# Kernel tuning notes

Hardware: AMD Instinct MI355X
Metric: run time of the kernel (lower is better)

Reference implementation:

```python
import jax, jax.numpy as jnp
import numpy as np

B, S, DIM = 2, 2048, 2048
N_HEADS, N_KV_HEADS = 16, 8
HEAD_DIM = DIM // N_HEADS          # 128
KV_DIM = N_KV_HEADS * HEAD_DIM     # 1024
SKETCH = 64
ROPE_THETA = 500000.0
INV_SQRT_HD = np.float32(1.0 / np.sqrt(HEAD_DIM))


def sketch_mm(A, Sm, Bm):
    """projection_sketch_mm: approximate A @ Bm as (A S / k) @ (S^T B).
    A: (b, n, d), Sm: (b, d, k), Bm: (d, m)."""
    AS = jnp.matmul(A, Sm) / Sm.shape[-1]      # (b, n, k)
    SB = jnp.einsum('bdk,dm->bkm', Sm, Bm)     # (b, k, m)
    return jnp.matmul(AS, SB)                  # (b, n, m)


def apply_rotary(x, freqs_cis):
    """Faithful port of the module's apply_rotary_emb for one tensor.
    x: (b, s, h, hd); freqs_cis: (s, hd//2, 2) with [...,0]=cos, [...,1]=sin."""
    x2 = x.reshape(*x.shape[:-1], HEAD_DIM // 2, 2)
    f = freqs_cis[None, :, None, :, :]         # broadcast over batch & heads
    c, s = f[..., 0], f[..., 1]
    x0, x1 = x2[..., 0], x2[..., 1]
    row1 = x0 * c + x1 * s                     # dot(x, [cos, sin])
    row0 = x0 * s - x1 * c                     # dot(x, [sin, -cos]) (flip + negate)
    return jnp.stack([row0, row1], axis=-1).reshape(x.shape)


def setup_inputs() -> dict:
    key = jax.random.key(0)
    ks = jax.random.split(key, 9)
    x = jax.random.normal(ks[0], (B, S, DIM), jnp.float32)
    wq = jax.random.normal(ks[1], (DIM, DIM), jnp.float32) / np.float32(np.sqrt(DIM))
    wk = jax.random.normal(ks[2], (KV_DIM, DIM), jnp.float32) / np.float32(np.sqrt(DIM))
    wv = jax.random.normal(ks[3], (KV_DIM, DIM), jnp.float32) / np.float32(np.sqrt(DIM))
    wo = jax.random.normal(ks[4], (DIM, DIM), jnp.float32) / np.float32(np.sqrt(DIM))
    # gaussian sketch matrices (sketch_mode='gaussian'), one per batch element
    Sq = jax.random.normal(ks[5], (B, DIM, SKETCH), jnp.float32)
    Sk = jax.random.normal(ks[6], (B, DIM, SKETCH), jnp.float32)
    Sv = jax.random.normal(ks[7], (B, DIM, SKETCH), jnp.float32)
    So = jax.random.normal(ks[8], (B, DIM, SKETCH), jnp.float32)
    # RoPE table: (S, HEAD_DIM//2, 2) = stack([cos, sin])
    pos = jnp.arange(S, dtype=jnp.float32)
    inv = 1.0 / (ROPE_THETA ** (jnp.arange(0, HEAD_DIM, 2, dtype=jnp.float32) / HEAD_DIM))
    ang = pos[:, None] * inv[None, :]
    freqs_cis = jnp.stack([jnp.cos(ang), jnp.sin(ang)], axis=-1)
    return {"x": x, "wq": wq, "wk": wk, "wv": wv, "wo": wo,
            "Sq": Sq, "Sk": Sk, "Sv": Sv, "So": So, "freqs_cis": freqs_cis}


def reference(x, wq, wk, wv, wo, Sq, Sk, Sv, So, freqs_cis):
    b, s, _ = x.shape
    # RLALinear projections via projection sketch (weight stored (out, in) -> use W.T)
    xq = sketch_mm(x, Sq, wq.T).reshape(b, s, N_HEADS, HEAD_DIM)
    xk = sketch_mm(x, Sk, wk.T).reshape(b, s, N_KV_HEADS, HEAD_DIM)
    xv = sketch_mm(x, Sv, wv.T).reshape(b, s, N_KV_HEADS, HEAD_DIM)
    xq = apply_rotary(xq, freqs_cis)
    xk = apply_rotary(xk, freqs_cis)
    # repeat_kv: each kv head repeated n_rep times consecutively
    n_rep = N_HEADS // N_KV_HEADS
    k = jnp.repeat(xk, n_rep, axis=2)
    v = jnp.repeat(xv, n_rep, axis=2)
    q = xq.transpose(0, 2, 1, 3)               # (b, h, s, d)
    k = k.transpose(0, 2, 1, 3)
    v = v.transpose(0, 2, 1, 3)
    scores = jnp.einsum('bhqd,bhkd->bhqk', q, k) * INV_SQRT_HD
    mask = jnp.tril(jnp.ones((s, s), dtype=bool))
    scores = jnp.where(mask[None, None], scores, jnp.finfo(scores.dtype).min)
    probs = jax.nn.softmax(scores, axis=-1)
    out = jnp.einsum('bhqk,bhkd->bhqd', probs, v)
    out = out.transpose(0, 2, 1, 3).reshape(b, s, DIM)
    # output RLALinear via sketch
    return sketch_mm(out, So, wo.T)
```

## Files before the change

### kernel.cpp

```cpp
#include <hip/hip_runtime.h>
#include <math.h>

#define S_LEN 2048
#define DIM   2048
#define NH    16
#define NKV   8
#define HD    128
#define SKETCH 64
#define KV_DIM 1024
#define SCALE (0.08838834764831845f * 1.4426950408889634f)

typedef _Float16 half8_t  __attribute__((ext_vector_type(8)));
typedef __bf16   bf8_t    __attribute__((ext_vector_type(8)));
typedef __bf16   bf4_t    __attribute__((ext_vector_type(4)));
typedef float    f32x16_t __attribute__((ext_vector_type(16)));
typedef unsigned int uint4_t __attribute__((ext_vector_type(4)));

__global__ __launch_bounds__(256) void sbas_mfma(
    const float* __restrict__ x,
    const float* __restrict__ Sq, const float* __restrict__ Sk,
    const float* __restrict__ Sv, const float* __restrict__ So,
    const float* __restrict__ wq, const float* __restrict__ wk,
    const float* __restrict__ wv, const float* __restrict__ wo,
    float* __restrict__ SBq, float* __restrict__ SBk,
    float* __restrict__ SBv, float* __restrict__ SBo,
    float* __restrict__ ASq, float* __restrict__ ASk,
    float* __restrict__ ASv) {
  __shared__ __align__(16) char smem[55296];
  const int tid = threadIdx.x, ln = tid & 63, w = tid >> 6;
  const int l31 = ln & 31, h32 = ln >> 5;
  const int bx = blockIdx.x;

  if (bx < 384) {
    const int bt = bx % 96, kc = bx / 96;
    const float *Ss, *W;
    float* SB;
    int Mout, n0;
    if (bt < 32)      { Ss = Sq; W = wq; SB = SBq; Mout = DIM;    n0 = bt * 64; }
    else if (bt < 48) { Ss = Sk; W = wk; SB = SBk; Mout = KV_DIM; n0 = (bt - 32) * 64; }
    else if (bt < 64) { Ss = Sv; W = wv; SB = SBv; Mout = KV_DIM; n0 = (bt - 48) * 64; }
    else              { Ss = So; W = wo; SB = SBo; Mout = DIM;    n0 = (bt - 64) * 64; }

    __bf16* Sth = (__bf16*)smem;
    __bf16* Stl = Sth + 9216;
    __bf16* Wh  = Stl + 9216;
    __bf16* Wl  = Wh + 4608;

    const int bw = w >> 1, mt = w & 1;
    f32x16_t acc[2];
#pragma unroll
    for (int ns = 0; ns < 2; ++ns)
#pragma unroll
      for (int r = 0; r < 16; ++r) acc[ns][r] = 0.0f;

    const int dbeg = kc * 512;
    for (int d0 = dbeg; d0 < dbeg + 512; d0 += 64) {
#pragma unroll
      for (int it = 0; it < 8; ++it) {
        int i = tid + it * 256;
        int b2 = i >> 10, rem = i & 1023;
        int d = rem >> 4, c4 = (rem & 15) << 2;
        float4 v = *(const float4*)(Ss + ((size_t)b2 * DIM + d0 + d) * SKETCH + c4);
        float vv[4] = {v.x, v.y, v.z, v.w};
#pragma unroll
        for (int j = 0; j < 4; ++j) {
          __bf16 hh = (__bf16)vv[j];
          Sth[(b2 * 64 + c4 + j) * 72 + d] = hh;
          Stl[(b2 * 64 + c4 + j) * 72 + d] = (__bf16)(vv[j] - (float)hh);
        }
      }
#pragma unroll
      for (int it = 0; it < 4; ++it) {
        int i = tid + it * 256;
        int c = i >> 4, d4 = (i & 15) << 2;
        float4 v = *(const float4*)(W + (size_t)(n0 + c) * DIM + d0 + d4);
        bf4_t hx, lx;
        float vv[4] = {v.x, v.y, v.z, v.w};
#pragma unroll
        for (int j = 0; j < 4; ++j) {
          __bf16 hh = (__bf16)vv[j];
          hx[j] = hh; lx[j] = (__bf16)(vv[j] - (float)hh);
        }
        *(bf4_t*)&Wh[c * 72 + d4] = hx;
        *(bf4_t*)&Wl[c * 72 + d4] = lx;
      }
      __syncthreads();
#pragma unroll
      for (int ks = 0; ks < 4; ++ks) {
        bf8_t ah = *(const bf8_t*)&Sth[(bw * 64 + mt * 32 + l31) * 72 + ks * 16 + h32 * 8];
        bf8_t al = *(const bf8_t*)&Stl[(bw * 64 + mt * 32 + l31) * 72 + ks * 16 + h32 * 8];
#pragma unroll
        for (int ns = 0; ns < 2; ++ns) {
          bf8_t bh_ = *(const bf8_t*)&Wh[(ns * 32 + l31) * 72 + ks * 16 + h32 * 8];
          bf8_t bl_ = *(const bf8_t*)&Wl[(ns * 32 + l31) * 72 + ks * 16 + h32 * 8];
          acc[ns] = __builtin_amdgcn_mfma_f32_32x32x16_bf16(ah, bh_, acc[ns], 0, 0, 0);
          acc[ns] = __builtin_amdgcn_mfma_f32_32x32x16_bf16(al, bh_, acc[ns], 0, 0, 0);
          acc[ns] = __builtin_amdgcn_mfma_f32_32x32x16_bf16(ah, bl_, acc[ns], 0, 0, 0);
        }
      }
      __syncthreads();
    }
#pragma unroll
    for (int ns = 0; ns < 2; ++ns)
#pragma unroll
      for (int r = 0; r < 16; ++r) {
        int kk = mt * 32 + (r & 3) + 8 * (r >> 2) + 4 * h32;
        atomicAdd(&SB[((size_t)bw * SKETCH + kk) * Mout + n0 + ns * 32 + l31], acc[ns][r]);
      }
  } else {
    const int idx = bx - 384;
    const int rt = idx >> 3, kc = idx & 7;
    const int row0 = rt * 128;
    const int bb = row0 >> 11;

    __bf16* Xh  = (__bf16*)smem;
    __bf16* Xl  = Xh + 9216;
    __bf16* S2h = Xl + 9216;
    __bf16* S2l = S2h + 4608;

    const float* Sp[3] = {Sq + (size_t)bb * DIM * SKETCH,
                          Sk + (size_t)bb * DIM * SKETCH,
                          Sv + (size_t)bb * DIM * SKETCH};
    float* Op[3] = {ASq, ASk, ASv};

    f32x16_t acc[3][2];
#pragma unroll
    for (int t = 0; t < 3; ++t)
#pragma unroll
      for (int nt = 0; nt < 2; ++nt)
#pragma unroll
        for (int r = 0; r < 16; ++r) acc[t][nt][r] = 0.0f;

    const int kbeg = kc * 256;
    for (int k0 = kbeg; k0 < kbeg + 256; k0 += 64) {
#pragma unroll
      for (int it = 0; it < 8; ++it) {
        int i = tid + it * 256;
        int r = i >> 4, c4 = (i & 15) << 2;
        float4 v = *(const float4*)(x + (size_t)(row0 + r) * DIM + k0 + c4);
        bf4_t hx, lx;
        float vv[4] = {v.x, v.y, v.z, v.w};
#pragma unroll
        for (int j = 0; j < 4; ++j) {
          __bf16 hh = (__bf16)vv[j];
          hx[j] = hh; lx[j] = (__bf16)(vv[j] - (float)hh);
        }
        *(bf4_t*)&Xh[r * 72 + c4] = hx;
        *(bf4_t*)&Xl[r * 72 + c4] = lx;
      }
#pragma unroll
      for (int t = 0; t < 3; ++t) {
#pragma unroll
        for (int it = 0; it < 4; ++it) {
          int i = tid + it * 256;
          int r = i & 63, c4 = (i >> 6) << 2;
          float4 v = *(const float4*)(Sp[t] + (size_t)(k0 + r) * SKETCH + c4);
          float vv[4] = {v.x, v.y, v.z, v.w};
#pragma unroll
          for (int j = 0; j < 4; ++j) {
            __bf16 hh = (__bf16)vv[j];
            S2h[(c4 + j) * 72 + r] = hh;
            S2l[(c4 + j) * 72 + r] = (__bf16)(vv[j] - (float)hh);
          }
        }
        __syncthreads();
#pragma unroll
        for (int ks = 0; ks < 4; ++ks) {
          bf8_t ah = *(const bf8_t*)&Xh[(w * 32 + l31) * 72 + ks * 16 + h32 * 8];
          bf8_t al = *(const bf8_t*)&Xl[(w * 32 + l31) * 72 + ks * 16 + h32 * 8];
#pragma unroll
          for (int nt = 0; nt < 2; ++nt) {
            bf8_t bh_ = *(const bf8_t*)&S2h[(nt * 32 + l31) * 72 + ks * 16 + h32 * 8];
            bf8_t bl_ = *(const bf8_t*)&S2l[(nt * 32 + l31) * 72 + ks * 16 + h32 * 8];
            acc[t][nt] = __builtin_amdgcn_mfma_f32_32x32x16_bf16(ah, bh_, acc[t][nt], 0, 0, 0);
            acc[t][nt] = __builtin_amdgcn_mfma_f32_32x32x16_bf16(al, bh_, acc[t][nt], 0, 0, 0);
            acc[t][nt] = __builtin_amdgcn_mfma_f32_32x32x16_bf16(ah, bl_, acc[t][nt], 0, 0, 0);
          }
        }
        __syncthreads();
      }
    }
#pragma unroll
    for (int t = 0; t < 3; ++t)
#pragma unroll
      for (int nt = 0; nt < 2; ++nt)
#pragma unroll
        for (int r = 0; r < 16; ++r) {
          int row = row0 + w * 32 + (r & 3) + 8 * (r >> 2) + 4 * h32;
          atomicAdd(&Op[t][(size_t)row * SKETCH + nt * 32 + l31],
                    acc[t][nt][r] * (1.0f / 64.0f));
        }
  }
}

__global__ __launch_bounds__(256) void as_mfma(
    const float* __restrict__ X, const float* __restrict__ S,
    float* __restrict__ OUT) {
  const int rt = blockIdx.x, kc = blockIdx.y;
  const int row0 = rt * 128;
  const int bb = row0 >> 11;
  const float* Sb = S + (size_t)bb * DIM * SKETCH;
  const int tid = threadIdx.x, ln = tid & 63, w = tid >> 6;
  const int l31 = ln & 31, h32 = ln >> 5;

  __shared__ __bf16 Xh[128][72], Xl[128][72];
  __shared__ __bf16 Sth[64][72], Stl[64][72];

  f32x16_t acc[2];
#pragma unroll
  for (int nt = 0; nt < 2; ++nt)
#pragma unroll
    for (int r = 0; r < 16; ++r) acc[nt][r] = 0.0f;

  const int kbeg = kc * 256;
  for (int k0 = kbeg; k0 < kbeg + 256; k0 += 64) {
#pragma unroll
    for (int it = 0; it < 8; ++it) {
      int idx = tid + it * 256;
      int r = idx >> 4, c4 = (idx & 15) << 2;
      float4 v = *(const float4*)(X + (size_t)(row0 + r) * DIM + k0 + c4);
      bf4_t hx, lx;
      float vv[4] = {v.x, v.y, v.z, v.w};
#pragma unroll
      for (int j = 0; j < 4; ++j) {
        __bf16 hh = (__bf16)vv[j];
        hx[j] = hh; lx[j] = (__bf16)(vv[j] - (float)hh);
      }
      *(bf4_t*)&Xh[r][c4] = hx;
      *(bf4_t*)&Xl[r][c4] = lx;
    }
#pragma unroll
    for (int it = 0; it < 4; ++it) {
      int idx = tid + it * 256;
      int r = idx & 63, c4 = (idx >> 6) << 2;
      float4 v = *(const float4*)(Sb + (size_t)(k0 + r) * SKETCH + c4);
      float vv[4] = {v.x, v.y, v.z, v.w};
#pragma unroll
      for (int j = 0; j < 4; ++j) {
        __bf16 hh = (__bf16)vv[j];
        Sth[c4 + j][r] = hh;
        Stl[c4 + j][r] = (__bf16)(vv[j] - (float)hh);
      }
    }
    __syncthreads();
#pragma unroll
    for (int ks = 0; ks < 4; ++ks) {
      bf8_t ah = *(const bf8_t*)&Xh[w * 32 + l31][ks * 16 + h32 * 8];
      bf8_t al = *(const bf8_t*)&Xl[w * 32 + l31][ks * 16 + h32 * 8];
#pragma unroll
      for (int nt = 0; nt < 2; ++nt) {
        bf8_t bh_ = *(const bf8_t*)&Sth[nt * 32 + l31][ks * 16 + h32 * 8];
        bf8_t bl_ = *(const bf8_t*)&Stl[nt * 32 + l31][ks * 16 + h32 * 8];
        acc[nt] = __builtin_amdgcn_mfma_f32_32x32x16_bf16(ah, bh_, acc[nt], 0, 0, 0);
        acc[nt] = __builtin_amdgcn_mfma_f32_32x32x16_bf16(al, bh_, acc[nt], 0, 0, 0);
        acc[nt] = __builtin_amdgcn_mfma_f32_32x32x16_bf16(ah, bl_, acc[nt], 0, 0, 0);
      }
    }
    __syncthreads();
  }
#pragma unroll
  for (int nt = 0; nt < 2; ++nt)
#pragma unroll
    for (int r = 0; r < 16; ++r) {
      int row = row0 + w * 32 + (r & 3) + 8 * (r >> 2) + 4 * h32;
      atomicAdd(&OUT[(size_t)row * SKETCH + nt * 32 + l31],
                acc[nt][r] * (1.0f / 64.0f));
    }
}

__device__ __forceinline__ void proj_gemm_core(
    const float* __restrict__ ASb, const float* __restrict__ SBb, int Mout,
    int s0, int n0, __bf16* ASh, __bf16* ASl, __bf16* SBth, __bf16* SBtl,
    f32x16_t acc[2]) {
  const int tid = threadIdx.x, ln = tid & 63, w = tid >> 6;
  const int l31 = ln & 31, h32 = ln >> 5;
#pragma unroll
  for (int it = 0; it < 8; ++it) {
    int i = tid + it * 256;
    int r = i >> 4, c4 = (i & 15) << 2;
    float4 v = *(const float4*)(ASb + (size_t)(s0 + r) * SKETCH + c4);
    bf4_t hx, lx;
    float vv[4] = {v.x, v.y, v.z, v.w};
#pragma unroll
    for (int j = 0; j < 4; ++j) {
      __bf16 hh = (__bf16)vv[j];
      hx[j] = hh; lx[j] = (__bf16)(vv[j] - (float)hh);
    }
    *(bf4_t*)&ASh[r * 72 + c4] = hx;
    *(bf4_t*)&ASl[r * 72 + c4] = lx;
  }
#pragma unroll
  for (int it = 0; it < 4; ++it) {
    int i = tid + it * 256;
    int k = i >> 4, c4 = (i & 15) << 2;
    float4 v = *(const float4*)(SBb + (size_t)k * Mout + n0 + c4);
    float vv[4] = {v.x, v.y, v.z, v.w};
#pragma unroll
    for (int j = 0; j < 4; ++j) {
      __bf16 hh = (__bf16)vv[j];
      SBth[(c4 + j) * 72 + k] = hh;
      SBtl[(c4 + j) * 72 + k] = (__bf16)(vv[j] - (float)hh);
    }
  }
  __syncthreads();
#pragma unroll
  for (int ks = 0; ks < 4; ++ks) {
    bf8_t ah = *(const bf8_t*)&ASh[(w * 32 + l31) * 72 + ks * 16 + h32 * 8];
    bf8_t al = *(const bf8_t*)&ASl[(w * 32 + l31) * 72 + ks * 16 + h32 * 8];
#pragma unroll
    for (int nt = 0; nt < 2; ++nt) {
      bf8_t bh_ = *(const bf8_t*)&SBth[(nt * 32 + l31) * 72 + ks * 16 + h32 * 8];
      bf8_t bl_ = *(const bf8_t*)&SBtl[(nt * 32 + l31) * 72 + ks * 16 + h32 * 8];
      acc[nt] = __builtin_amdgcn_mfma_f32_32x32x16_bf16(ah, bh_, acc[nt], 0, 0, 0);
      acc[nt] = __builtin_amdgcn_mfma_f32_32x32x16_bf16(al, bh_, acc[nt], 0, 0, 0);
      acc[nt] = __builtin_amdgcn_mfma_f32_32x32x16_bf16(ah, bl_, acc[nt], 0, 0, 0);
    }
  }
}

__global__ __launch_bounds__(256) void proj_qkv(
    const float* __restrict__ ASq, const float* __restrict__ ASk,
    const float* __restrict__ ASv,
    const float* __restrict__ SBq, const float* __restrict__ SBk,
    const float* __restrict__ SBv,
    const float* __restrict__ freqs,
    _Float16* __restrict__ Qf, _Float16* __restrict__ Kf,
    _Float16* __restrict__ Vf) {
  __shared__ __bf16 ASh[128 * 72], ASl[128 * 72], SBth[64 * 72], SBtl[64 * 72];
  const int b = blockIdx.z, y = blockIdx.y;
  const float *AS, *SB;
  int Mout, nh, mt;
  _Float16* OUT;
  bool rope;
  if (y < 32)      { AS = ASq; SB = SBq; Mout = DIM;    nh = NH;  mt = y;      OUT = Qf; rope = true; }
  else if (y < 48) { AS = ASk; SB = SBk; Mout = KV_DIM; nh = NKV; mt = y - 32; OUT = Kf; rope = true; }
  else             { AS = ASv; SB = SBv; Mout = KV_DIM; nh = NKV; mt = y - 48; OUT = Vf; rope = false; }
  const int s0 = blockIdx.x * 128, n0 = mt * 64;
  f32x16_t acc[2];
#pragma unroll
  for (int nt = 0; nt < 2; ++nt)
#pragma unroll
    for (int r = 0; r < 16; ++r) acc[nt][r] = 0.0f;
  proj_gemm_core(AS + (size_t)b * S_LEN * SKETCH, SB + (size_t)b * SKETCH * Mout,
                 Mout, s0, n0, ASh, ASl, SBth, SBtl, acc);
  const int tid = threadIdx.x, ln = tid & 63, w = tid >> 6;
  const int l31 = ln & 31, h32 = ln >> 5;
  const bool meven = (l31 & 1) == 0;
#pragma unroll
  for (int nt = 0; nt < 2; ++nt) {
    const int m = n0 + nt * 32 + l31;
    const int h = m >> 7, hd = m & (HD - 1);
    const int p = hd >> 1;
#pragma unroll
    for (int r = 0; r < 16; ++r) {
      const int s = s0 + w * 32 + (r & 3) + 8 * (r >> 2) + 4 * h32;
      float v = acc[nt][r];
      float outv;
      if (rope) {
        int pi = __builtin_bit_cast(int, v);
        float part = __builtin_bit_cast(float, __builtin_amdgcn_ds_swizzle(pi, 0x041F));
        float co = freqs[((size_t)s * 64 + p) * 2 + 0];
        float si = freqs[((size_t)s * 64 + p) * 2 + 1];
        outv = meven ? (v * si - part * co) : (part * co + v * si);
      } else {
        outv = v;
      }
      OUT[(((size_t)b * nh + h) * S_LEN + s) * HD + hd] = (_Float16)outv;
    }
  }
}

__global__ __launch_bounds__(256) void proj_out(
    const float* __restrict__ ASo, const float* __restrict__ SBo,
    float* __restrict__ out) {
  __shared__ __bf16 ASh[128 * 72], ASl[128 * 72], SBth[64 * 72], SBtl[64 * 72];
  const int b = blockIdx.z;
  const int s0 = blockIdx.x * 128, n0 = blockIdx.y * 64;
  f32x16_t acc[2];
#pragma unroll
  for (int nt = 0; nt < 2; ++nt)
#pragma unroll
    for (int r = 0; r < 16; ++r) acc[nt][r] = 0.0f;
  proj_gemm_core(ASo + (size_t)b * S_LEN * SKETCH, SBo + (size_t)b * SKETCH * DIM,
                 DIM, s0, n0, ASh, ASl, SBth, SBtl, acc);
  const int tid = threadIdx.x, ln = tid & 63, w = tid >> 6;
  const int l31 = ln & 31, h32 = ln >> 5;
#pragma unroll
  for (int nt = 0; nt < 2; ++nt)
#pragma unroll
    for (int r = 0; r < 16; ++r) {
      const int s = s0 + w * 32 + (r & 3) + 8 * (r >> 2) + 4 * h32;
      out[((size_t)b * S_LEN + s) * DIM + n0 + nt * 32 + l31] = acc[nt][r];
    }
}

#define QTT 128
#define KTT 64
#define KP  136
#define VP  72

__global__ __launch_bounds__(256, 2) void attn_mfma(
    const _Float16* __restrict__ Qf, const _Float16* __restrict__ Kf,
    const _Float16* __restrict__ Vf, float* __restrict__ O) {
  const int bh = blockIdx.y;
  const int b = bh >> 4, h = bh & 15, g = h >> 1;
  const int qt = 15 - (int)blockIdx.x;
  const int q0 = qt * QTT;

  const int tid = threadIdx.x;
  const int ln = tid & 63, w = tid >> 6;
  const int l31 = ln & 31, h32 = ln >> 5;
  const bool hb = (h32 != 0);

  __shared__ _Float16 Ks[KTT][KP];
  __shared__ _Float16 Vts[HD][VP];
  float* Ot = (float*)&Vts[0][0];

  const _Float16* Kp = Kf + (size_t)(b * NKV + g) * S_LEN * HD;
  const _Float16* Vp = Vf + (size_t)(b * NKV + g) * S_LEN * HD;

  half8_t qfr[8];
  {
    const size_t qrow = (size_t)(b * NH + h) * S_LEN + q0 + w * 32 + l31;
#pragma unroll
    for (int ks = 0; ks < 8; ++ks)
      qfr[ks] = *(const half8_t*)(Qf + qrow * HD + ks * 16 + h32 * 8);
  }

  float mrow = -1.0e30f, lrow = 0.0f;
  f32x16_t o[4];
#pragma unroll
  for (int dt = 0; dt < 4; ++dt)
#pragma unroll
    for (int r = 0; r < 16; ++r) o[dt][r] = 0.0f;

  const int wq_start = q0 + w * 32;
  const int qq = wq_start + l31;
  const int nkt = 2 * qt + 2;

  half8_t kreg[4], vreg[4];
#pragma unroll
  for (int it = 0; it < 4; ++it) {
    int i = tid + it * 256;
    kreg[it] = *(const half8_t*)(Kp + (size_t)(i >> 4) * HD + ((i & 15) << 3));
    vreg[it] = *(const half8_t*)(Vp + (size_t)(i & 63) * HD + (((i >> 6) << 3)));
  }
#pragma unroll
  for (int it = 0; it < 4; ++it) {
    int i = tid + it * 256;
    *(half8_t*)&Ks[i >> 4][(i & 15) << 3] = kreg[it];
    int k = i & 63, d0 = (i >> 6) << 3;
#pragma unroll
    for (int j = 0; j < 8; ++j) Vts[d0 + j][k] = vreg[it][j];
  }
  __syncthreads();

  for (int kt = 0; kt < nkt; ++kt) {
    const int k0 = kt * KTT;
    if (kt + 1 < nkt) {
      const int kn = k0 + KTT;
#pragma unroll
      for (int it = 0; it < 4; ++it) {
        int i = tid + it * 256;
        kreg[it] = *(const half8_t*)(Kp + (size_t)(kn + (i >> 4)) * HD + ((i & 15) << 3));
        vreg[it] = *(const half8_t*)(Vp + (size_t)(kn + (i & 63)) * HD + (((i >> 6) << 3)));
      }
    }

    if (k0 < wq_start + 32) {
      f32x16_t sc[2];
#pragma unroll
      for (int nt = 0; nt < 2; ++nt)
#pragma unroll
        for (int r = 0; r < 16; ++r) sc[nt][r] = 0.0f;
#pragma unroll
      for (int ks = 0; ks < 8; ++ks)
#pragma unroll
        for (int nt = 0; nt < 2; ++nt) {
          half8_t kf = *(const half8_t*)&Ks[nt * 32 + l31][ks * 16 + h32 * 8];
          sc[nt] = __builtin_amdgcn_mfma_f32_32x32x16_f16(kf, qfr[ks], sc[nt], 0, 0, 0);
        }
      const bool needMask = (k0 + KTT > wq_start);
#pragma unroll
      for (int nt = 0; nt < 2; ++nt)
#pragma unroll
        for (int r = 0; r < 16; ++r) {
          int kg = k0 + nt * 32 + (r & 3) + 8 * (r >> 2) + 4 * h32;
          float s = sc[nt][r] * SCALE;
          sc[nt][r] = (!needMask || kg <= qq) ? s : -1.0e30f;
        }
      float ml = sc[0][0];
#pragma unroll
      for (int r = 1; r < 16; ++r) ml = fmaxf(ml, sc[0][r]);
#pragma unroll
      for (int r = 0; r < 16; ++r) ml = fmaxf(ml, sc[1][r]);
      ml = fmaxf(ml, __shfl_xor(ml, 32));
      float mn = fmaxf(mrow, ml);
      float alpha = __builtin_amdgcn_exp2f(mrow - mn);
      mrow = mn;
      float ps = 0.0f;
#pragma unroll
      for (int nt = 0; nt < 2; ++nt)
#pragma unroll
        for (int r = 0; r < 16; ++r) {
          float p = __builtin_amdgcn_exp2f(sc[nt][r] - mn);
          sc[nt][r] = p;
          ps += p;
        }
      ps += __shfl_xor(ps, 32);
      lrow = lrow * alpha + ps;
#pragma unroll
      for (int dt = 0; dt < 4; ++dt)
#pragma unroll
        for (int r = 0; r < 16; ++r) o[dt][r] *= alpha;

      unsigned int pk[2][8];
#pragma unroll
      for (int nt = 0; nt < 2; ++nt)
#pragma unroll
        for (int gq = 0; gq < 8; ++gq)
          pk[nt][gq] = __builtin_bit_cast(
              unsigned int,
              __builtin_amdgcn_cvt_pkrtz(sc[nt][2 * gq], sc[nt][2 * gq + 1]));
#pragma unroll
      for (int ks2 = 0; ks2 < 4; ++ks2) {
        const int nt = ks2 >> 1, a = ks2 & 1;
        unsigned int own0 = hb ? pk[nt][4 * a + 2] : pk[nt][4 * a + 0];
        unsigned int own1 = hb ? pk[nt][4 * a + 3] : pk[nt][4 * a + 1];
        unsigned int oth0 = hb ? pk[nt][4 * a + 0] : pk[nt][4 * a + 2];
        unsigned int oth1 = hb ? pk[nt][4 * a + 1] : pk[nt][4 * a + 3];
        unsigned int rcv0 = __shfl_xor(oth0, 32);
        unsigned int rcv1 = __shfl_xor(oth1, 32);
        uint4_t fu;
        fu.x = hb ? rcv0 : own0;
        fu.y = hb ? rcv1 : own1;
        fu.z = hb ? own0 : rcv0;
        fu.w = hb ? own1 : rcv1;
        half8_t pf = __builtin_bit_cast(half8_t, fu);
#pragma unroll
        for (int dt = 0; dt < 4; ++dt) {
          half8_t vf = *(const half8_t*)&Vts[dt * 32 + l31][ks2 * 16 + h32 * 8];
          o[dt] = __builtin_amdgcn_mfma_f32_32x32x16_f16(vf, pf, o[dt], 0, 0, 0);
        }
      }
    }

    if (kt + 1 < nkt) {
      __syncthreads();
#pragma unroll
      for (int it = 0; it < 4; ++it) {
        int i = tid + it * 256;
        *(half8_t*)&Ks[i >> 4][(i & 15) << 3] = kreg[it];
        int k = i & 63, d0 = (i >> 6) << 3;
#pragma unroll
        for (int j = 0; j < 8; ++j) Vts[d0 + j][k] = vreg[it][j];
      }
      __syncthreads();
    }
  }

  const float linv = 1.0f / lrow;
  const int s_l = tid >> 5, d_l = tid & 31;
#pragma unroll
  for (int dt = 0; dt < 4; ++dt) {
    __syncthreads();
#pragma unroll
    for (int gq = 0; gq < 4; ++gq) {
      float4 vv;
      vv.x = o[dt][4 * gq + 0] * linv;
      vv.y = o[dt][4 * gq + 1] * linv;
      vv.z = o[dt][4 * gq + 2] * linv;
      vv.w = o[dt][4 * gq + 3] * linv;
      *(float4*)&Ot[(w * 32 + l31) * 36 + 8 * gq + 4 * h32] = vv;
    }
    __syncthreads();
#pragma unroll
    for (int i = 0; i < 16; ++i) {
      int s = s_l + 8 * i;
      float v = Ot[s * 36 + d_l];
      O[((size_t)b * S_LEN + q0 + s) * DIM + h * HD + dt * 32 + d_l] = v;
    }
  }
}

extern "C" void kernel_launch(void* const* d_in, const int* in_sizes, int n_in,
                              void* d_out, int out_size, void* d_ws, size_t ws_size,
                              hipStream_t stream) {
  const float* x     = (const float*)d_in[0];
  const float* wq    = (const float*)d_in[1];
  const float* wk    = (const float*)d_in[2];
  const float* wv    = (const float*)d_in[3];
  const float* wo    = (const float*)d_in[4];
  const float* Sq    = (const float*)d_in[5];
  const float* Sk    = (const float*)d_in[6];
  const float* Sv    = (const float*)d_in[7];
  const float* So    = (const float*)d_in[8];
  const float* freqs = (const float*)d_in[9];
  float* out = (float*)d_out;

  const size_t AS_E = (size_t)2 * S_LEN * SKETCH;
  const size_t SBQ_E = (size_t)2 * SKETCH * DIM;
  const size_t SBK_E = (size_t)2 * SKETCH * KV_DIM;

  float* fp = (float*)d_ws;
  float* ASq = fp;  fp += AS_E;
  float* ASk = fp;  fp += AS_E;
  float* ASv = fp;  fp += AS_E;
  float* ASo = fp;  fp += AS_E;
  float* SBq = fp;  fp += SBQ_E;
  float* SBk = fp;  fp += SBK_E;
  float* SBv = fp;  fp += SBK_E;
  float* SBo = fp;  fp += SBQ_E;
  float* ATT = fp;  fp += (size_t)2 * S_LEN * DIM;
  _Float16* hp = (_Float16*)fp;
  _Float16* Qfb = hp; hp += (size_t)2 * NH  * S_LEN * HD;
  _Float16* Kfb = hp; hp += (size_t)2 * NKV * S_LEN * HD;
  _Float16* Vfb = hp; hp += (size_t)2 * NKV * S_LEN * HD;

  (void)hipMemsetAsync(ASq, 0, (4 * AS_E + 2 * SBQ_E + 2 * SBK_E) * sizeof(float), stream);

  hipLaunchKernelGGL(sbas_mfma, dim3(640), dim3(256), 0, stream,
                     x, Sq, Sk, Sv, So, wq, wk, wv, wo,
                     SBq, SBk, SBv, SBo, ASq, ASk, ASv);
  hipLaunchKernelGGL(proj_qkv, dim3(16, 64, 2), dim3(256), 0, stream,
                     ASq, ASk, ASv, SBq, SBk, SBv, freqs, Qfb, Kfb, Vfb);
  hipLaunchKernelGGL(attn_mfma, dim3(16, 32), dim3(256), 0, stream,
                     Qfb, Kfb, Vfb, ATT);
  hipLaunchKernelGGL(as_mfma, dim3(32, 8), dim3(256), 0, stream, ATT, So, ASo);
  hipLaunchKernelGGL(proj_out, dim3(16, 32, 2), dim3(256), 0, stream, ASo, SBo, out);
}
```

Baseline: 371.9 us.

## Split KV range across two wave groups per attention block and merge

Attention blocks grow to 512 threads. The two 256-thread halves each handle half of the causal KV tiles for the same 128-query tile, then merge their partial softmax state (max, sum, output) through shared memory. This doubles the waves working on each query tile and shortens the serial KV loop, which matters most for the long causal tiles. K is now read straight from global memory instead of being staged in LDS, which frees LDS for two V buffers but relies on cache hits for the repeated K fragment loads. The grid is also reordered so query tiles vary along y.

```diff
diff --git a/kernel.cpp b/kernel.cpp
--- a/kernel.cpp
+++ b/kernel.cpp
@@ -396,32 +396,32 @@
 
 #define QTT 128
 #define KTT 64
-#define KP  136
 #define VP  72
 
-__global__ __launch_bounds__(256, 2) void attn_mfma(
+__global__ __launch_bounds__(512, 4) void attn_mfma(
     const _Float16* __restrict__ Qf, const _Float16* __restrict__ Kf,
     const _Float16* __restrict__ Vf, float* __restrict__ O) {
-  const int bh = blockIdx.y;
+  const int bh = blockIdx.x;
   const int b = bh >> 4, h = bh & 15, g = h >> 1;
-  const int qt = 15 - (int)blockIdx.x;
+  const int qt = 15 - (int)blockIdx.y;
   const int q0 = qt * QTT;
 
   const int tid = threadIdx.x;
   const int ln = tid & 63, w = tid >> 6;
+  const int wg = w & 3, half = w >> 2;
   const int l31 = ln & 31, h32 = ln >> 5;
   const bool hb = (h32 != 0);
 
-  __shared__ _Float16 Ks[KTT][KP];
-  __shared__ _Float16 Vts[HD][VP];
-  float* Ot = (float*)&Vts[0][0];
+  __shared__ __align__(16) _Float16 Vts[2][HD][VP];
+  float* Pl = (float*)&Vts[0][0][0];
+  float* Ot = (float*)&Vts[0][0][0];
 
   const _Float16* Kp = Kf + (size_t)(b * NKV + g) * S_LEN * HD;
   const _Float16* Vp = Vf + (size_t)(b * NKV + g) * S_LEN * HD;
 
   half8_t qfr[8];
   {
-    const size_t qrow = (size_t)(b * NH + h) * S_LEN + q0 + w * 32 + l31;
+    const size_t qrow = (size_t)(b * NH + h) * S_LEN + q0 + wg * 32 + l31;
 #pragma unroll
     for (int ks = 0; ks < 8; ++ks)
       qfr[ks] = *(const half8_t*)(Qf + qrow * HD + ks * 16 + h32 * 8);
@@ -434,37 +434,43 @@
 #pragma unroll
     for (int r = 0; r < 16; ++r) o[dt][r] = 0.0f;
 
-  const int wq_start = q0 + w * 32;
+  const int wq_start = q0 + wg * 32;
   const int qq = wq_start + l31;
-  const int nkt = 2 * qt + 2;
-
-  half8_t kreg[4], vreg[4];
-#pragma unroll
-  for (int it = 0; it < 4; ++it) {
-    int i = tid + it * 256;
-    kreg[it] = *(const half8_t*)(Kp + (size_t)(i >> 4) * HD + ((i & 15) << 3));
-    vreg[it] = *(const half8_t*)(Vp + (size_t)(i & 63) * HD + (((i >> 6) << 3)));
-  }
-#pragma unroll
-  for (int it = 0; it < 4; ++it) {
-    int i = tid + it * 256;
-    *(half8_t*)&Ks[i >> 4][(i & 15) << 3] = kreg[it];
-    int k = i & 63, d0 = (i >> 6) << 3;
-#pragma unroll
-    for (int j = 0; j < 8; ++j) Vts[d0 + j][k] = vreg[it][j];
-  }
+  const int nsteps = qt + 1;
+  const int ktbase = half * nsteps;
+
+  half8_t vreg[2][2];
+#pragma unroll
+  for (int s = 0; s < 2; ++s)
+#pragma unroll
+    for (int it = 0; it < 2; ++it) {
+      int i2 = tid + it * 512;
+      int k = i2 & 63, d0 = (i2 >> 6) << 3;
+      vreg[s][it] = *(const half8_t*)(Vp + (size_t)(s * nsteps * 64 + k) * HD + d0);
+    }
+#pragma unroll
+  for (int s = 0; s < 2; ++s)
+#pragma unroll
+    for (int it = 0; it < 2; ++it) {
+      int i2 = tid + it * 512;
+      int k = i2 & 63, d0 = (i2 >> 6) << 3;
+#pragma unroll
+      for (int j = 0; j < 8; ++j) Vts[s][d0 + j][k] = vreg[s][it][j];
+    }
   __syncthreads();
 
-  for (int kt = 0; kt < nkt; ++kt) {
+  for (int i = 0; i < nsteps; ++i) {
+    const int kt = ktbase + i;
     const int k0 = kt * KTT;
-    if (kt + 1 < nkt) {
-      const int kn = k0 + KTT;
-#pragma unroll
-      for (int it = 0; it < 4; ++it) {
-        int i = tid + it * 256;
-        kreg[it] = *(const half8_t*)(Kp + (size_t)(kn + (i >> 4)) * HD + ((i & 15) << 3));
-        vreg[it] = *(const half8_t*)(Vp + (size_t)(kn + (i & 63)) * HD + (((i >> 6) << 3)));
-      }
+    if (i + 1 < nsteps) {
+#pragma unroll
+      for (int s = 0; s < 2; ++s)
+#pragma unroll
+        for (int it = 0; it < 2; ++it) {
+          int i2 = tid + it * 512;
+          int k = i2 & 63, d0 = (i2 >> 6) << 3;
+          vreg[s][it] = *(const half8_t*)(Vp + (size_t)((s * nsteps + i + 1) * 64 + k) * HD + d0);
+        }
     }
 
     if (k0 < wq_start + 32) {
@@ -477,7 +483,7 @@
       for (int ks = 0; ks < 8; ++ks)
 #pragma unroll
         for (int nt = 0; nt < 2; ++nt) {
-          half8_t kf = *(const half8_t*)&Ks[nt * 32 + l31][ks * 16 + h32 * 8];
+          half8_t kf = *(const half8_t*)(Kp + (size_t)(k0 + nt * 32 + l31) * HD + ks * 16 + h32 * 8);
           sc[nt] = __builtin_amdgcn_mfma_f32_32x32x16_f16(kf, qfr[ks], sc[nt], 0, 0, 0);
         }
       const bool needMask = (k0 + KTT > wq_start);
@@ -539,24 +545,82 @@
         half8_t pf = __builtin_bit_cast(half8_t, fu);
 #pragma unroll
         for (int dt = 0; dt < 4; ++dt) {
-          half8_t vf = *(const half8_t*)&Vts[dt * 32 + l31][ks2 * 16 + h32 * 8];
+          half8_t vf = *(const half8_t*)&Vts[half][dt * 32 + l31][ks2 * 16 + h32 * 8];
           o[dt] = __builtin_amdgcn_mfma_f32_32x32x16_f16(vf, pf, o[dt], 0, 0, 0);
         }
       }
     }
 
-    if (kt + 1 < nkt) {
+    if (i + 1 < nsteps) {
       __syncthreads();
 #pragma unroll
-      for (int it = 0; it < 4; ++it) {
-        int i = tid + it * 256;
-        *(half8_t*)&Ks[i >> 4][(i & 15) << 3] = kreg[it];
-        int k = i & 63, d0 = (i >> 6) << 3;
-#pragma unroll
-        for (int j = 0; j < 8; ++j) Vts[d0 + j][k] = vreg[it][j];
-      }
+      for (int s = 0; s < 2; ++s)
+#pragma unroll
+        for (int it = 0; it < 2; ++it) {
+          int i2 = tid + it * 512;
+          int k = i2 & 63, d0 = (i2 >> 6) << 3;
+#pragma unroll
+          for (int j = 0; j < 8; ++j) Vts[s][d0 + j][k] = vreg[s][it][j];
+        }
       __syncthreads();
     }
+  }
+
+  __syncthreads();
+  if (w >= 4 && w < 6) {
+    float* dst = Pl + ((size_t)(w - 4) * 64 + ln) * 68;
+#pragma unroll
+    for (int dt = 0; dt < 4; ++dt)
+#pragma unroll
+      for (int gq = 0; gq < 4; ++gq) {
+        float4 vv;
+        vv.x = o[dt][4 * gq + 0]; vv.y = o[dt][4 * gq + 1];
+        vv.z = o[dt][4 * gq + 2]; vv.w = o[dt][4 * gq + 3];
+        *(float4*)&dst[dt * 16 + gq * 4] = vv;
+      }
+    dst[64] = mrow; dst[65] = lrow;
+  }
+  __syncthreads();
+  if (w < 2) {
+    const float* src = Pl + ((size_t)w * 64 + ln) * 68;
+    float m2 = src[64], l2 = src[65];
+    float mn = fmaxf(mrow, m2);
+    float a1 = __builtin_amdgcn_exp2f(mrow - mn);
+    float a2 = __builtin_amdgcn_exp2f(m2 - mn);
+    lrow = lrow * a1 + l2 * a2;
+#pragma unroll
+    for (int dt = 0; dt < 4; ++dt)
+#pragma unroll
+      for (int r = 0; r < 16; ++r)
+        o[dt][r] = o[dt][r] * a1 + src[dt * 16 + r] * a2;
+  }
+  __syncthreads();
+  if (w >= 6) {
+    float* dst = Pl + ((size_t)(w - 6) * 64 + ln) * 68;
+#pragma unroll
+    for (int dt = 0; dt < 4; ++dt)
+#pragma unroll
+      for (int gq = 0; gq < 4; ++gq) {
+        float4 vv;
+        vv.x = o[dt][4 * gq + 0]; vv.y = o[dt][4 * gq + 1];
+        vv.z = o[dt][4 * gq + 2]; vv.w = o[dt][4 * gq + 3];
+        *(float4*)&dst[dt * 16 + gq * 4] = vv;
+      }
+    dst[64] = mrow; dst[65] = lrow;
+  }
+  __syncthreads();
+  if (w >= 2 && w < 4) {
+    const float* src = Pl + ((size_t)(w - 2) * 64 + ln) * 68;
+    float m2 = src[64], l2 = src[65];
+    float mn = fmaxf(mrow, m2);
+    float a1 = __builtin_amdgcn_exp2f(mrow - mn);
+    float a2 = __builtin_amdgcn_exp2f(m2 - mn);
+    lrow = lrow * a1 + l2 * a2;
+#pragma unroll
+    for (int dt = 0; dt < 4; ++dt)
+#pragma unroll
+      for (int r = 0; r < 16; ++r)
+        o[dt][r] = o[dt][r] * a1 + src[dt * 16 + r] * a2;
   }
 
   const float linv = 1.0f / lrow;
@@ -564,19 +628,21 @@
 #pragma unroll
   for (int dt = 0; dt < 4; ++dt) {
     __syncthreads();
-#pragma unroll
-    for (int gq = 0; gq < 4; ++gq) {
-      float4 vv;
-      vv.x = o[dt][4 * gq + 0] * linv;
-      vv.y = o[dt][4 * gq + 1] * linv;
-      vv.z = o[dt][4 * gq + 2] * linv;
-      vv.w = o[dt][4 * gq + 3] * linv;
-      *(float4*)&Ot[(w * 32 + l31) * 36 + 8 * gq + 4 * h32] = vv;
+    if (w < 4) {
+#pragma unroll
+      for (int gq = 0; gq < 4; ++gq) {
+        float4 vv;
+        vv.x = o[dt][4 * gq + 0] * linv;
+        vv.y = o[dt][4 * gq + 1] * linv;
+        vv.z = o[dt][4 * gq + 2] * linv;
+        vv.w = o[dt][4 * gq + 3] * linv;
+        *(float4*)&Ot[(wg * 32 + l31) * 36 + 8 * gq + 4 * h32] = vv;
+      }
     }
     __syncthreads();
 #pragma unroll
-    for (int i = 0; i < 16; ++i) {
-      int s = s_l + 8 * i;
+    for (int i = 0; i < 8; ++i) {
+      int s = s_l + 16 * i;
       float v = Ot[s * 36 + d_l];
       O[((size_t)b * S_LEN + q0 + s) * DIM + h * HD + dt * 32 + d_l] = v;
     }
@@ -624,7 +690,7 @@
                      SBq, SBk, SBv, SBo, ASq, ASk, ASv);
   hipLaunchKernelGGL(proj_qkv, dim3(16, 64, 2), dim3(256), 0, stream,
                      ASq, ASk, ASv, SBq, SBk, SBv, freqs, Qfb, Kfb, Vfb);
-  hipLaunchKernelGGL(attn_mfma, dim3(16, 32), dim3(256), 0, stream,
+  hipLaunchKernelGGL(attn_mfma, dim3(32, 16), dim3(512), 0, stream,
                      Qfb, Kfb, Vfb, ATT);
   hipLaunchKernelGGL(as_mfma, dim3(32, 8), dim3(256), 0, stream, ATT, So, ASo);
   hipLaunchKernelGGL(proj_out, dim3(16, 32, 2), dim3(256), 0, stream, ASo, SBo, out);
```

Measured after the change: 482.8 us. 1.3x slower.

## Split attention KV range across wave pairs with flash-decoding style merge

Applied to the files above, without the earlier changes.

The attention kernel now uses 64-row query tiles, with the grid changed to (32,32) and heads on x. Within a block, two wave pairs each process half of the causal KV tiles in separate shared-memory buffers. Their partial softmax states are merged through LDS at the end. K and transposed-V tiles also get an XOR-swizzled LDS layout to reduce bank conflicts. The aim is more parallelism and better load balance across the causal triangle, at the cost of a 64KB shared buffer that may limit occupancy, extra merge work, and Q fragments loaded twice per block.

```diff
diff --git a/kernel.cpp b/kernel.cpp
--- a/kernel.cpp
+++ b/kernel.cpp
@@ -394,34 +394,34 @@
     }
 }
 
-#define QTT 128
 #define KTT 64
-#define KP  136
-#define VP  72
 
 __global__ __launch_bounds__(256, 2) void attn_mfma(
     const _Float16* __restrict__ Qf, const _Float16* __restrict__ Kf,
     const _Float16* __restrict__ Vf, float* __restrict__ O) {
-  const int bh = blockIdx.y;
+  const int bh = blockIdx.x;
   const int b = bh >> 4, h = bh & 15, g = h >> 1;
-  const int qt = 15 - (int)blockIdx.x;
-  const int q0 = qt * QTT;
+  const int qt = 31 - (int)blockIdx.y;
+  const int q0 = qt * 64;
 
   const int tid = threadIdx.x;
   const int ln = tid & 63, w = tid >> 6;
+  const int wg = w & 1, half = w >> 1;
   const int l31 = ln & 31, h32 = ln >> 5;
   const bool hb = (h32 != 0);
 
-  __shared__ _Float16 Ks[KTT][KP];
-  __shared__ _Float16 Vts[HD][VP];
-  float* Ot = (float*)&Vts[0][0];
+  __shared__ __align__(16) char smem[65536];
+  char* KsH = smem + half * 16384;
+  char* VtH = smem + 32768 + half * 16384;
+  float* Pl = (float*)smem;
+  float* Ot = (float*)smem;
 
   const _Float16* Kp = Kf + (size_t)(b * NKV + g) * S_LEN * HD;
   const _Float16* Vp = Vf + (size_t)(b * NKV + g) * S_LEN * HD;
 
   half8_t qfr[8];
   {
-    const size_t qrow = (size_t)(b * NH + h) * S_LEN + q0 + w * 32 + l31;
+    const size_t qrow = (size_t)(b * NH + h) * S_LEN + q0 + wg * 32 + l31;
 #pragma unroll
     for (int ks = 0; ks < 8; ++ks)
       qfr[ks] = *(const half8_t*)(Qf + qrow * HD + ks * 16 + h32 * 8);
@@ -434,40 +434,58 @@
 #pragma unroll
     for (int r = 0; r < 16; ++r) o[dt][r] = 0.0f;
 
-  const int wq_start = q0 + w * 32;
+  const int wq_start = q0 + wg * 32;
   const int qq = wq_start + l31;
-  const int nkt = 2 * qt + 2;
-
-  half8_t kreg[4], vreg[4];
-#pragma unroll
-  for (int it = 0; it < 4; ++it) {
-    int i = tid + it * 256;
-    kreg[it] = *(const half8_t*)(Kp + (size_t)(i >> 4) * HD + ((i & 15) << 3));
-    vreg[it] = *(const half8_t*)(Vp + (size_t)(i & 63) * HD + (((i >> 6) << 3)));
-  }
-#pragma unroll
-  for (int it = 0; it < 4; ++it) {
-    int i = tid + it * 256;
-    *(half8_t*)&Ks[i >> 4][(i & 15) << 3] = kreg[it];
-    int k = i & 63, d0 = (i >> 6) << 3;
-#pragma unroll
-    for (int j = 0; j < 8; ++j) Vts[d0 + j][k] = vreg[it][j];
-  }
+  const int nkt = qt + 1;
+  const int nk0 = (nkt + 1) >> 1, nk1 = nkt >> 1;
+
+  half8_t kregA[4], vregA[4], kregB[4], vregB[4];
+
+#define LOADK(dst, t)                                                          \
+  _Pragma("unroll") for (int it_ = 0; it_ < 4; ++it_) {                        \
+    int i_ = tid + it_ * 256;                                                  \
+    dst[it_] = *(const half8_t*)(Kp + (size_t)((t) * 64 + (i_ >> 4)) * HD +    \
+                                 ((i_ & 15) << 3));                            \
+  }
+#define LOADV(dst, t)                                                          \
+  _Pragma("unroll") for (int it_ = 0; it_ < 4; ++it_) {                        \
+    int i_ = tid + it_ * 256;                                                  \
+    dst[it_] = *(const half8_t*)(Vp + (size_t)((t) * 64 + (i_ & 63)) * HD +    \
+                                 ((i_ >> 6) << 3));                            \
+  }
+#define STOREK(base, src)                                                      \
+  _Pragma("unroll") for (int it_ = 0; it_ < 4; ++it_) {                        \
+    int i_ = tid + it_ * 256;                                                  \
+    int row_ = i_ >> 4, gg_ = (i_ & 15) ^ (row_ & 15);                         \
+    *(half8_t*)((base) + row_ * 256 + (gg_ << 4)) = src[it_];                  \
+  }
+#define STOREV(base, src)                                                      \
+  _Pragma("unroll") for (int it_ = 0; it_ < 4; ++it_) {                        \
+    int i_ = tid + it_ * 256;                                                  \
+    int k_ = i_ & 63, d0_ = (i_ >> 6) << 3;                                    \
+    _Pragma("unroll") for (int j_ = 0; j_ < 8; ++j_) {                         \
+      int d_ = d0_ + j_, gg_ = (k_ >> 3) ^ (d_ & 7);                           \
+      *(_Float16*)((base) + d_ * 128 + (gg_ << 4) + ((k_ & 7) << 1)) =         \
+          src[it_][j_];                                                        \
+    }                                                                          \
+  }
+
+  LOADK(kregA, 0); LOADV(vregA, 0);
+  if (nk1 > 0) { LOADK(kregB, nk0); LOADV(vregB, nk0); }
+  STOREK(smem, kregA); STOREV(smem + 32768, vregA);
+  if (nk1 > 0) { STOREK(smem + 16384, kregB); STOREV(smem + 49152, vregB); }
   __syncthreads();
 
-  for (int kt = 0; kt < nkt; ++kt) {
-    const int k0 = kt * KTT;
-    if (kt + 1 < nkt) {
-      const int kn = k0 + KTT;
-#pragma unroll
-      for (int it = 0; it < 4; ++it) {
-        int i = tid + it * 256;
-        kreg[it] = *(const half8_t*)(Kp + (size_t)(kn + (i >> 4)) * HD + ((i & 15) << 3));
-        vreg[it] = *(const half8_t*)(Vp + (size_t)(kn + (i & 63)) * HD + (((i >> 6) << 3)));
-      }
-    }
-
-    if (k0 < wq_start + 32) {
+  for (int i = 0; i < nk0; ++i) {
+    const bool pfA = (i + 1 < nk0), pfB = (i + 1 < nk1);
+    if (pfA) { LOADK(kregA, i + 1); LOADV(vregA, i + 1); }
+    if (pfB) { LOADK(kregB, nk0 + i + 1); LOADV(vregB, nk0 + i + 1); }
+
+    const int myt = half ? (nk0 + i) : i;
+    const int k0 = myt * KTT;
+    const bool active = (half ? (i < nk1) : true) && (k0 < wq_start + 32);
+
+    if (active) {
       f32x16_t sc[2];
 #pragma unroll
       for (int nt = 0; nt < 2; ++nt)
@@ -477,7 +495,9 @@
       for (int ks = 0; ks < 8; ++ks)
 #pragma unroll
         for (int nt = 0; nt < 2; ++nt) {
-          half8_t kf = *(const half8_t*)&Ks[nt * 32 + l31][ks * 16 + h32 * 8];
+          const int kk = nt * 32 + l31;
+          half8_t kf = *(const half8_t*)(
+              KsH + kk * 256 + ((((ks << 1) + h32) ^ (kk & 15)) << 4));
           sc[nt] = __builtin_amdgcn_mfma_f32_32x32x16_f16(kf, qfr[ks], sc[nt], 0, 0, 0);
         }
       const bool needMask = (k0 + KTT > wq_start);
@@ -539,24 +559,49 @@
         half8_t pf = __builtin_bit_cast(half8_t, fu);
 #pragma unroll
         for (int dt = 0; dt < 4; ++dt) {
-          half8_t vf = *(const half8_t*)&Vts[dt * 32 + l31][ks2 * 16 + h32 * 8];
+          const int d = dt * 32 + l31;
+          half8_t vf = *(const half8_t*)(
+              VtH + d * 128 + ((((ks2 << 1) + h32) ^ (d & 7)) << 4));
           o[dt] = __builtin_amdgcn_mfma_f32_32x32x16_f16(vf, pf, o[dt], 0, 0, 0);
         }
       }
     }
 
-    if (kt + 1 < nkt) {
+    if (pfA || pfB) {
       __syncthreads();
-#pragma unroll
-      for (int it = 0; it < 4; ++it) {
-        int i = tid + it * 256;
-        *(half8_t*)&Ks[i >> 4][(i & 15) << 3] = kreg[it];
-        int k = i & 63, d0 = (i >> 6) << 3;
-#pragma unroll
-        for (int j = 0; j < 8; ++j) Vts[d0 + j][k] = vreg[it][j];
-      }
+      if (pfA) { STOREK(smem, kregA); STOREV(smem + 32768, vregA); }
+      if (pfB) { STOREK(smem + 16384, kregB); STOREV(smem + 49152, vregB); }
       __syncthreads();
     }
+  }
+
+  __syncthreads();
+  if (w >= 2) {
+    float* dst = Pl + ((size_t)(w - 2) * 64 + ln) * 68;
+#pragma unroll
+    for (int dt = 0; dt < 4; ++dt)
+#pragma unroll
+      for (int gq = 0; gq < 4; ++gq) {
+        float4 vv;
+        vv.x = o[dt][4 * gq + 0]; vv.y = o[dt][4 * gq + 1];
+        vv.z = o[dt][4 * gq + 2]; vv.w = o[dt][4 * gq + 3];
+        *(float4*)&dst[dt * 16 + gq * 4] = vv;
+      }
+    dst[64] = mrow; dst[65] = lrow;
+  }
+  __syncthreads();
+  if (w < 2) {
+    const float* src = Pl + ((size_t)w * 64 + ln) * 68;
+    float m2 = src[64], l2 = src[65];
+    float mn = fmaxf(mrow, m2);
+    float a1 = __builtin_amdgcn_exp2f(mrow - mn);
+    float a2 = __builtin_amdgcn_exp2f(m2 - mn);
+    lrow = lrow * a1 + l2 * a2;
+#pragma unroll
+    for (int dt = 0; dt < 4; ++dt)
+#pragma unroll
+      for (int r = 0; r < 16; ++r)
+        o[dt][r] = o[dt][r] * a1 + src[dt * 16 + r] * a2;
   }
 
   const float linv = 1.0f / lrow;
@@ -564,23 +609,29 @@
 #pragma unroll
   for (int dt = 0; dt < 4; ++dt) {
     __syncthreads();
-#pragma unroll
-    for (int gq = 0; gq < 4; ++gq) {
-      float4 vv;
-      vv.x = o[dt][4 * gq + 0] * linv;
-      vv.y = o[dt][4 * gq + 1] * linv;
-      vv.z = o[dt][4 * gq + 2] * linv;
-      vv.w = o[dt][4 * gq + 3] * linv;
-      *(float4*)&Ot[(w * 32 + l31) * 36 + 8 * gq + 4 * h32] = vv;
+    if (w < 2) {
+#pragma unroll
+      for (int gq = 0; gq < 4; ++gq) {
+        float4 vv;
+        vv.x = o[dt][4 * gq + 0] * linv;
+        vv.y = o[dt][4 * gq + 1] * linv;
+        vv.z = o[dt][4 * gq + 2] * linv;
+        vv.w = o[dt][4 * gq + 3] * linv;
+        *(float4*)&Ot[(wg * 32 + l31) * 36 + 8 * gq + 4 * h32] = vv;
+      }
     }
     __syncthreads();
 #pragma unroll
-    for (int i = 0; i < 16; ++i) {
+    for (int i = 0; i < 8; ++i) {
       int s = s_l + 8 * i;
       float v = Ot[s * 36 + d_l];
       O[((size_t)b * S_LEN + q0 + s) * DIM + h * HD + dt * 32 + d_l] = v;
     }
   }
+#undef LOADK
+#undef LOADV
+#undef STOREK
+#undef STOREV
 }
 
 extern "C" void kernel_launch(void* const* d_in, const int* in_sizes, int n_in,
@@ -624,7 +675,7 @@
                      SBq, SBk, SBv, SBo, ASq, ASk, ASv);
   hipLaunchKernelGGL(proj_qkv, dim3(16, 64, 2), dim3(256), 0, stream,
                      ASq, ASk, ASv, SBq, SBk, SBv, freqs, Qfb, Kfb, Vfb);
-  hipLaunchKernelGGL(attn_mfma, dim3(16, 32), dim3(256), 0, stream,
+  hipLaunchKernelGGL(attn_mfma, dim3(32, 32), dim3(256), 0, stream,
                      Qfb, Kfb, Vfb, ATT);
   hipLaunchKernelGGL(as_mfma, dim3(32, 8), dim3(256), 0, stream, ATT, So, ASo);
   hipLaunchKernelGGL(proj_out, dim3(16, 32, 2), dim3(256), 0, stream, ASo, SBo, out);
```

After: 396.6 us. 6.6% more time.

## Fuse output sketch projection into attention epilogue, drop ATT buffer

Applied to the files above, without the earlier changes.

The attention kernel now multiplies its normalized per-head output tile by the matching 128-row slice of So with fp16 MFMA, then atomically accumulates into ASo. This removes the separate as_mfma kernel and the full fp32 attention output write and re-read. In exchange it adds 16 heads' worth of atomic contention per ASo element and lowers the So and attention-output precision from a split-bf16 pair to single fp16, which could affect accuracy.

```diff
diff --git a/kernel.cpp b/kernel.cpp
--- a/kernel.cpp
+++ b/kernel.cpp
@@ -191,81 +191,6 @@
                     acc[t][nt][r] * (1.0f / 64.0f));
         }
   }
-}
-
-__global__ __launch_bounds__(256) void as_mfma(
-    const float* __restrict__ X, const float* __restrict__ S,
-    float* __restrict__ OUT) {
-  const int rt = blockIdx.x, kc = blockIdx.y;
-  const int row0 = rt * 128;
-  const int bb = row0 >> 11;
-  const float* Sb = S + (size_t)bb * DIM * SKETCH;
-  const int tid = threadIdx.x, ln = tid & 63, w = tid >> 6;
-  const int l31 = ln & 31, h32 = ln >> 5;
-
-  __shared__ __bf16 Xh[128][72], Xl[128][72];
-  __shared__ __bf16 Sth[64][72], Stl[64][72];
-
-  f32x16_t acc[2];
-#pragma unroll
-  for (int nt = 0; nt < 2; ++nt)
-#pragma unroll
-    for (int r = 0; r < 16; ++r) acc[nt][r] = 0.0f;
-
-  const int kbeg = kc * 256;
-  for (int k0 = kbeg; k0 < kbeg + 256; k0 += 64) {
-#pragma unroll
-    for (int it = 0; it < 8; ++it) {
-      int idx = tid + it * 256;
-      int r = idx >> 4, c4 = (idx & 15) << 2;
-      float4 v = *(const float4*)(X + (size_t)(row0 + r) * DIM + k0 + c4);
-      bf4_t hx, lx;
-      float vv[4] = {v.x, v.y, v.z, v.w};
-#pragma unroll
-      for (int j = 0; j < 4; ++j) {
-        __bf16 hh = (__bf16)vv[j];
-        hx[j] = hh; lx[j] = (__bf16)(vv[j] - (float)hh);
-      }
-      *(bf4_t*)&Xh[r][c4] = hx;
-      *(bf4_t*)&Xl[r][c4] = lx;
-    }
-#pragma unroll
-    for (int it = 0; it < 4; ++it) {
-      int idx = tid + it * 256;
-      int r = idx & 63, c4 = (idx >> 6) << 2;
-      float4 v = *(const float4*)(Sb + (size_t)(k0 + r) * SKETCH + c4);
-      float vv[4] = {v.x, v.y, v.z, v.w};
-#pragma unroll
-      for (int j = 0; j < 4; ++j) {
-        __bf16 hh = (__bf16)vv[j];
-        Sth[c4 + j][r] = hh;
-        Stl[c4 + j][r] = (__bf16)(vv[j] - (float)hh);
-      }
-    }
-    __syncthreads();
-#pragma unroll
-    for (int ks = 0; ks < 4; ++ks) {
-      bf8_t ah = *(const bf8_t*)&Xh[w * 32 + l31][ks * 16 + h32 * 8];
-      bf8_t al = *(const bf8_t*)&Xl[w * 32 + l31][ks * 16 + h32 * 8];
-#pragma unroll
-      for (int nt = 0; nt < 2; ++nt) {
-        bf8_t bh_ = *(const bf8_t*)&Sth[nt * 32 + l31][ks * 16 + h32 * 8];
-        bf8_t bl_ = *(const bf8_t*)&Stl[nt * 32 + l31][ks * 16 + h32 * 8];
-        acc[nt] = __builtin_amdgcn_mfma_f32_32x32x16_bf16(ah, bh_, acc[nt], 0, 0, 0);
-        acc[nt] = __builtin_amdgcn_mfma_f32_32x32x16_bf16(al, bh_, acc[nt], 0, 0, 0);
-        acc[nt] = __builtin_amdgcn_mfma_f32_32x32x16_bf16(ah, bl_, acc[nt], 0, 0, 0);
-      }
-    }
-    __syncthreads();
-  }
-#pragma unroll
-  for (int nt = 0; nt < 2; ++nt)
-#pragma unroll
-    for (int r = 0; r < 16; ++r) {
-      int row = row0 + w * 32 + (r & 3) + 8 * (r >> 2) + 4 * h32;
-      atomicAdd(&OUT[(size_t)row * SKETCH + nt * 32 + l31],
-                acc[nt][r] * (1.0f / 64.0f));
-    }
 }
 
 __device__ __forceinline__ void proj_gemm_core(
@@ -401,7 +326,8 @@
 
 __global__ __launch_bounds__(256, 2) void attn_mfma(
     const _Float16* __restrict__ Qf, const _Float16* __restrict__ Kf,
-    const _Float16* __restrict__ Vf, float* __restrict__ O) {
+    const _Float16* __restrict__ Vf, const float* __restrict__ So,
+    float* __restrict__ ASo) {
   const int bh = blockIdx.y;
   const int b = bh >> 4, h = bh & 15, g = h >> 1;
   const int qt = 15 - (int)blockIdx.x;
@@ -414,7 +340,6 @@
 
   __shared__ _Float16 Ks[KTT][KP];
   __shared__ _Float16 Vts[HD][VP];
-  float* Ot = (float*)&Vts[0][0];
 
   const _Float16* Kp = Kf + (size_t)(b * NKV + g) * S_LEN * HD;
   const _Float16* Vp = Vf + (size_t)(b * NKV + g) * S_LEN * HD;
@@ -560,26 +485,69 @@
   }
 
   const float linv = 1.0f / lrow;
-  const int s_l = tid >> 5, d_l = tid & 31;
-#pragma unroll
-  for (int dt = 0; dt < 4; ++dt) {
-    __syncthreads();
-#pragma unroll
-    for (int gq = 0; gq < 4; ++gq) {
-      float4 vv;
-      vv.x = o[dt][4 * gq + 0] * linv;
-      vv.y = o[dt][4 * gq + 1] * linv;
-      vv.z = o[dt][4 * gq + 2] * linv;
-      vv.w = o[dt][4 * gq + 3] * linv;
-      *(float4*)&Ot[(w * 32 + l31) * 36 + 8 * gq + 4 * h32] = vv;
-    }
-    __syncthreads();
-#pragma unroll
-    for (int i = 0; i < 16; ++i) {
-      int s = s_l + 8 * i;
-      float v = Ot[s * 36 + d_l];
-      O[((size_t)b * S_LEN + q0 + s) * DIM + h * HD + dt * 32 + d_l] = v;
-    }
+  __syncthreads();
+  {
+    const float* Sop = So + ((size_t)b * DIM + h * HD) * SKETCH;
+    _Float16* SoT = &Ks[0][0];
+#pragma unroll
+    for (int it = 0; it < 8; ++it) {
+      int i = tid + it * 256;
+      int r = i >> 4, c4 = (i & 15) << 2;
+      float4 v = *(const float4*)(Sop + (size_t)r * SKETCH + c4);
+      SoT[(c4 + 0) * KP + r] = (_Float16)v.x;
+      SoT[(c4 + 1) * KP + r] = (_Float16)v.y;
+      SoT[(c4 + 2) * KP + r] = (_Float16)v.z;
+      SoT[(c4 + 3) * KP + r] = (_Float16)v.w;
+    }
+  }
+  __syncthreads();
+  f32x16_t ca[2];
+#pragma unroll
+  for (int nt = 0; nt < 2; ++nt)
+#pragma unroll
+    for (int r = 0; r < 16; ++r) ca[nt][r] = 0.0f;
+  {
+    const _Float16* SoT = &Ks[0][0];
+#pragma unroll
+    for (int ks8 = 0; ks8 < 8; ++ks8) {
+      const int dt = ks8 >> 1, c = ks8 & 1;
+      unsigned int pw0 = __builtin_bit_cast(unsigned int,
+          __builtin_amdgcn_cvt_pkrtz(o[dt][8 * c + 0] * linv, o[dt][8 * c + 1] * linv));
+      unsigned int pw1 = __builtin_bit_cast(unsigned int,
+          __builtin_amdgcn_cvt_pkrtz(o[dt][8 * c + 2] * linv, o[dt][8 * c + 3] * linv));
+      unsigned int pw2 = __builtin_bit_cast(unsigned int,
+          __builtin_amdgcn_cvt_pkrtz(o[dt][8 * c + 4] * linv, o[dt][8 * c + 5] * linv));
+      unsigned int pw3 = __builtin_bit_cast(unsigned int,
+          __builtin_amdgcn_cvt_pkrtz(o[dt][8 * c + 6] * linv, o[dt][8 * c + 7] * linv));
+      unsigned int own0 = hb ? pw2 : pw0;
+      unsigned int own1 = hb ? pw3 : pw1;
+      unsigned int oth0 = hb ? pw0 : pw2;
+      unsigned int oth1 = hb ? pw1 : pw3;
+      unsigned int rcv0 = __shfl_xor(oth0, 32);
+      unsigned int rcv1 = __shfl_xor(oth1, 32);
+      uint4_t fu;
+      fu.x = hb ? rcv0 : own0;
+      fu.y = hb ? rcv1 : own1;
+      fu.z = hb ? own0 : rcv0;
+      fu.w = hb ? own1 : rcv1;
+      half8_t bfv = __builtin_bit_cast(half8_t, fu);
+#pragma unroll
+      for (int nt = 0; nt < 2; ++nt) {
+        half8_t af = *(const half8_t*)&SoT[(nt * 32 + l31) * KP + ks8 * 16 + h32 * 8];
+        ca[nt] = __builtin_amdgcn_mfma_f32_32x32x16_f16(af, bfv, ca[nt], 0, 0, 0);
+      }
+    }
+  }
+  {
+    const int q = q0 + w * 32 + l31;
+    float* ASob = ASo + (size_t)b * S_LEN * SKETCH;
+#pragma unroll
+    for (int nt = 0; nt < 2; ++nt)
+#pragma unroll
+      for (int r = 0; r < 16; ++r) {
+        int k = nt * 32 + (r & 3) + 8 * (r >> 2) + 4 * h32;
+        atomicAdd(&ASob[(size_t)q * SKETCH + k], ca[nt][r] * (1.0f / 64.0f));
+      }
   }
 }
 
@@ -611,7 +579,6 @@
   float* SBk = fp;  fp += SBK_E;
   float* SBv = fp;  fp += SBK_E;
   float* SBo = fp;  fp += SBQ_E;
-  float* ATT = fp;  fp += (size_t)2 * S_LEN * DIM;
   _Float16* hp = (_Float16*)fp;
   _Float16* Qfb = hp; hp += (size_t)2 * NH  * S_LEN * HD;
   _Float16* Kfb = hp; hp += (size_t)2 * NKV * S_LEN * HD;
@@ -625,7 +592,6 @@
   hipLaunchKernelGGL(proj_qkv, dim3(16, 64, 2), dim3(256), 0, stream,
                      ASq, ASk, ASv, SBq, SBk, SBv, freqs, Qfb, Kfb, Vfb);
   hipLaunchKernelGGL(attn_mfma, dim3(16, 32), dim3(256), 0, stream,
-                     Qfb, Kfb, Vfb, ATT);
-  hipLaunchKernelGGL(as_mfma, dim3(32, 8), dim3(256), 0, stream, ATT, So, ASo);
+                     Qfb, Kfb, Vfb, So, ASo);
   hipLaunchKernelGGL(proj_out, dim3(16, 32, 2), dim3(256), 0, stream, ASo, SBo, out);
 }
```

Measured after the change: 375.9 us. Within noise of the previous version (+1.1%).
